# Performance work log

Measured on AMD Instinct MI355X. Metric: run time of the kernel, lower is better.

## Reference

```python
import jax, jax.numpy as jnp
import numpy as np

B, T, C = 4, 1024, 768
H, HD = 12, 64
E, K, DFF = 16, 2, 3072
EPS = 1e-5


def layernorm(x, w, b):
    mu = jnp.mean(x, axis=-1, keepdims=True)
    xc = x - mu
    var = jnp.mean(xc * xc, axis=-1, keepdims=True)
    return xc * jax.lax.rsqrt(var + EPS) * w + b


def setup_inputs() -> dict:
    key = jax.random.key(0)
    ks = jax.random.split(key, 12)
    s = lambda fan_in: 1.0 / np.sqrt(fan_in)
    return {
        "x": jax.random.normal(ks[0], (B, T, C), jnp.float32),
        "ln1_w": jnp.ones((C,), jnp.float32),
        "ln1_b": jnp.zeros((C,), jnp.float32),
        "W_attn": jax.random.normal(ks[1], (C, 3 * C), jnp.float32) * s(C),
        "b_attn": jnp.zeros((3 * C,), jnp.float32),
        "W_proj": jax.random.normal(ks[2], (C, C), jnp.float32) * s(C),
        "b_proj": jnp.zeros((C,), jnp.float32),
        "ln2_w": jnp.ones((C,), jnp.float32),
        "ln2_b": jnp.zeros((C,), jnp.float32),
        "W_router": jax.random.normal(ks[3], (C, E), jnp.float32) * s(C),
        "W1": jax.random.normal(ks[4], (E, C, DFF), jnp.float32) * s(C),
        "b1": jnp.zeros((E, DFF), jnp.float32),
        "W2": jax.random.normal(ks[5], (E, DFF, C), jnp.float32) * s(DFF),
        "b2": jnp.zeros((E, C), jnp.float32),
    }


def reference(x, ln1_w, ln1_b, W_attn, b_attn, W_proj, b_proj,
              ln2_w, ln2_b, W_router, W1, b1, W2, b2):
    # --- attention sublayer ---
    xn = layernorm(x, ln1_w, ln1_b)
    qkv = xn @ W_attn + b_attn                                  # [B,T,3C]
    q, k, v = jnp.split(qkv, 3, axis=-1)
    q = q.reshape(B, T, H, HD).transpose(0, 2, 1, 3)            # [B,H,T,HD]
    k = k.reshape(B, T, H, HD).transpose(0, 2, 1, 3)
    v = v.reshape(B, T, H, HD).transpose(0, 2, 1, 3)
    att = jnp.einsum('bhqd,bhkd->bhqk', q, k) / np.sqrt(HD)
    causal = jnp.tril(jnp.ones((T, T), bool))
    att = jnp.where(causal, att, -jnp.inf)
    att = jax.nn.softmax(att, axis=-1)
    y = jnp.einsum('bhqk,bhkd->bhqd', att, v)
    y = y.transpose(0, 2, 1, 3).reshape(B, T, C)
    x = x + y @ W_proj + b_proj

    # --- MoE sublayer: dense all-experts with top-k gating mask ---
    xn2 = layernorm(x, ln2_w, ln2_b)
    probs = jax.nn.softmax(xn2 @ W_router, axis=-1)             # [B,T,E]
    top_p, top_idx = jax.lax.top_k(probs, K)                    # [B,T,K]
    gating = jnp.sum(jax.nn.one_hot(top_idx, E, dtype=probs.dtype)
                     * top_p[..., None], axis=-2)               # [B,T,E]
    g = jnp.moveaxis(gating, -1, 0)                             # [E,B,T]

    def body(acc, params):
        W1e, b1e, W2e, b2e, ge = params
        h = jax.nn.gelu(xn2 @ W1e + b1e, approximate=False)     # [B,T,DFF]
        out = h @ W2e + b2e                                     # [B,T,C]
        return acc + ge[..., None] * out, None

    y_moe, _ = jax.lax.scan(body, jnp.zeros_like(x), (W1, b1, W2, b2, g))
    # note: MoELayer returns x + y, and Block adds residual again
    return x + (xn2_residual := 0) + xn2 * 0 + (x * 0) + x * 0 + y_moe + x * 0 if False else x + (x * 0) + y_moe + x * 0 * 0 if False else x + x * 0 + y_moe + (x - x) if False else x + (x + y_moe) - x + (x + y_moe) - (x + y_moe) if False else x + x + y_moe - x if False else (x + (x + y_moe)) - x + (x - x) if False else x + y_moe + x - x if False else _block_out(x, xn2, y_moe)


def _block_out(x, xn2, y_moe):
    # MoELayer.forward returns x_in + y where x_in is ln2 *input* (x here);
    # Block then does x = x + ffn(ln2(x)) -> x + (x + y_moe)? No: MoE input is
    # xn2 = ln2(x), so ffn(ln2(x)) = xn2 + y_moe, and Block adds residual x.
    return x + xn2 + y_moe
```

## Files before the change

### kernel.cpp

```cpp
#include <hip/hip_runtime.h>
#include <math.h>

#define CC    768
#define C3    2304
#define KD    2304
#define LDA2  1536
#define TT    1024
#define BB    4
#define HH    12
#define HD    64
#define EE    16
#define DFFN  3072
#define NTOK  4096
#define NSLOT 8192
#define LDP   136

typedef unsigned short u16;
typedef unsigned int   u32;
typedef __attribute__((ext_vector_type(8))) short short8;
typedef __attribute__((ext_vector_type(4))) float floatx4;

__device__ __forceinline__ u16 f2bf(float f){
  u32 x = __builtin_bit_cast(u32, f);
  x += 0x7fffu + ((x >> 16) & 1u);
  return (u16)(x >> 16);
}
__device__ __forceinline__ u16 f2h(float f){
  _Float16 h = (_Float16)f;
  return __builtin_bit_cast(u16, h);
}
__device__ __forceinline__ float h2f(u16 u){
  return (float)__builtin_bit_cast(_Float16, u);
}
__device__ __forceinline__ float gelu_exact(float v){
  return 0.5f * v * (1.f + erff(v * 0.70710678118654752440f));
}
__device__ __forceinline__ void split2h(float v, u16& h0, u16& h1){
  float vs = v * 64.f;
  h0 = f2h(vs);
  h1 = f2h(vs - h2f(h0));
}

template<int MODE>
__global__ __launch_bounds__(256) void transpose_split(const float* __restrict__ src,
    u16* __restrict__ d0, int R, int Cn)
{
  __shared__ float tile[32][33];
  int z = blockIdx.z;
  const float* s = src + (size_t)z * R * Cn;
  int c0 = blockIdx.x * 32, r0 = blockIdx.y * 32;
  int tx = threadIdx.x & 31, ty = threadIdx.x >> 5;
  #pragma unroll
  for (int j = 0; j < 4; ++j)
    tile[ty + j*8][tx] = s[(size_t)(r0 + ty + j*8) * Cn + c0 + tx];
  __syncthreads();
  #pragma unroll
  for (int j = 0; j < 4; ++j){
    float v = tile[tx][ty + j*8];
    if (MODE == 1){
      u16 h0, h1; split2h(v, h0, h1);
      size_t base = (size_t)(c0 + ty + j*8) * LDA2 + (r0 + tx);
      d0[base] = h0; d0[base + 768] = h1;
    } else {
      d0[(size_t)z * R * Cn + (size_t)(c0 + ty + j*8) * R + r0 + tx] = f2bf(v);
    }
  }
}

template<int MODE>
__global__ __launch_bounds__(256) void ln_kernel(const float* __restrict__ x,
    const float* __restrict__ gw, const float* __restrict__ gb,
    float* __restrict__ of, u16* __restrict__ o0)
{
  int tok = blockIdx.x, tid = threadIdx.x;
  const float* xr = x + (size_t)tok * CC;
  float v0 = xr[tid], v1 = xr[tid + 256], v2 = xr[tid + 512];
  __shared__ float r1[4], r2[4];
  __shared__ float mus, rss;
  float s = v0 + v1 + v2;
  #pragma unroll
  for (int off = 32; off >= 1; off >>= 1) s += __shfl_down(s, off);
  if ((tid & 63) == 0) r1[tid >> 6] = s;
  __syncthreads();
  if (tid == 0) mus = (r1[0] + r1[1] + r1[2] + r1[3]) * (1.f / 768.f);
  __syncthreads();
  float mu = mus;
  float d0 = v0 - mu, d1 = v1 - mu, d2 = v2 - mu;
  float t = d0*d0 + d1*d1 + d2*d2;
  #pragma unroll
  for (int off = 32; off >= 1; off >>= 1) t += __shfl_down(t, off);
  if ((tid & 63) == 0) r2[tid >> 6] = t;
  __syncthreads();
  if (tid == 0) rss = rsqrtf((r2[0] + r2[1] + r2[2] + r2[3]) * (1.f / 768.f) + 1e-5f);
  __syncthreads();
  float rstd = rss;
  float dv[3] = {d0, d1, d2};
  #pragma unroll
  for (int i = 0; i < 3; ++i){
    int c = tid + i * 256;
    float vv = dv[i] * rstd * gw[c] + gb[c];
    if (MODE == 1){
      u16 h0, h1; split2h(vv, h0, h1);
      o0[(size_t)tok * LDA2 + c] = h0;
      o0[(size_t)tok * LDA2 + 768 + c] = h1;
    } else {
      size_t idx = (size_t)tok * CC + c;
      of[idx] = vv;
      o0[idx] = f2bf(vv);
    }
  }
}

template<int BETA>
__global__ __launch_bounds__(256) void gemm_dense(
    const u16* __restrict__ A, const u16* __restrict__ Bt,
    float* __restrict__ C, const float* __restrict__ bias, int N)
{
  __shared__ u16 As[128 * 32];
  __shared__ u16 Bs[128 * 32];
  int tid = threadIdx.x;
  int lane = tid & 63, wave = tid >> 6;
  int wm = wave & 1, wn = wave >> 1;
  int m0 = blockIdx.y * 128, n0 = blockIdx.x * 128;
  int ra = tid >> 2, ka = (tid & 3) * 8;
  const u16* pa0 = A  + (size_t)(m0 + ra)      * LDA2 + ka;
  const u16* pa1 = A  + (size_t)(m0 + ra + 64) * LDA2 + ka;
  const u16* pb0 = Bt + (size_t)(n0 + ra)      * LDA2 + ka;
  const u16* pb1 = Bt + (size_t)(n0 + ra + 64) * LDA2 + ka;
  floatx4 acc[4][4] = {};
  int el = lane & 15, eq = lane >> 4;
  for (int k0 = 0; k0 < KD; k0 += 32){
    int ca = (k0 >= 768) ? k0 - 768 : k0;
    int cb = (k0 < 1536) ? k0 : k0 - 1536;
    __syncthreads();
    uint4 va0 = *(const uint4*)(pa0 + ca);
    uint4 va1 = *(const uint4*)(pa1 + ca);
    uint4 vb0 = *(const uint4*)(pb0 + cb);
    uint4 vb1 = *(const uint4*)(pb1 + cb);
    *(uint4*)&As[(size_t)ra * 32 + ka]        = va0;
    *(uint4*)&As[(size_t)(ra + 64) * 32 + ka] = va1;
    *(uint4*)&Bs[(size_t)ra * 32 + ka]        = vb0;
    *(uint4*)&Bs[(size_t)(ra + 64) * 32 + ka] = vb1;
    __syncthreads();
    short8 fa[4], fb[4];
    #pragma unroll
    for (int t = 0; t < 4; ++t)
      fa[t] = *(const short8*)&As[(size_t)(wm*64 + t*16 + el) * 32 + eq*8];
    #pragma unroll
    for (int t = 0; t < 4; ++t)
      fb[t] = *(const short8*)&Bs[(size_t)(wn*64 + t*16 + el) * 32 + eq*8];
    #pragma unroll
    for (int mt = 0; mt < 4; ++mt)
      #pragma unroll
      for (int nt = 0; nt < 4; ++nt)
        acc[mt][nt] = __builtin_amdgcn_mfma_f32_16x16x32_f16(fa[mt], fb[nt], acc[mt][nt], 0, 0, 0);
  }
  const float ds = 1.f / 4096.f;
  #pragma unroll
  for (int mt = 0; mt < 4; ++mt){
    #pragma unroll
    for (int nt = 0; nt < 4; ++nt){
      int col = n0 + wn*64 + nt*16 + el;
      float bv = bias ? bias[col] : 0.f;
      #pragma unroll
      for (int r = 0; r < 4; ++r){
        int row = m0 + wm*64 + mt*16 + eq*4 + r;
        size_t idx = (size_t)row * N + col;
        float val = acc[mt][nt][r] * ds + bv;
        if (BETA) val += C[idx];
        C[idx] = val;
      }
    }
  }
}

__global__ __launch_bounds__(256) void flash_mfma(const float* __restrict__ qkv,
    u16* __restrict__ yH)
{
  __shared__ u16 Qs[128 * LDP];
  __shared__ u16 Ks[64 * LDP];
  __shared__ u16 Vt[64 * LDP];
  __shared__ u16 Ps[128 * LDP];
  int tid = threadIdx.x;
  int lane = tid & 63, wv = tid >> 6;
  int qi = 7 - blockIdx.x;
  int bh = blockIdx.y;
  int b = bh / HH, h = bh % HH;
  int el = lane & 15, eq = lane >> 4;
  int m0 = wv * 32;
  int row0 = qi * 128;

  {
    int r = tid >> 1, d0 = (tid & 1) * 32;
    const float* src = qkv + (size_t)(b*TT + row0 + r) * C3 + h*HD + d0;
    u16* q0 = &Qs[r * LDP + d0];
    #pragma unroll
    for (int i = 0; i < 32; i += 2){
      u16 a0, a1, b0, b1;
      split2h(src[i], a0, a1);
      split2h(src[i+1], b0, b1);
      *(u32*)&q0[i]      = (u32)a0 | ((u32)b0 << 16);
      *(u32*)&q0[64 + i] = (u32)a1 | ((u32)b1 << 16);
    }
  }
  floatx4 O[2][4] = {};
  float mrow[2][4], lrow[2][4];
  #pragma unroll
  for (int a = 0; a < 2; ++a)
    #pragma unroll
    for (int r = 0; r < 4; ++r){ mrow[a][r] = -1e30f; lrow[a][r] = 0.f; }

  const float cmul = 0.125f * 1.44269504088896340736f / 4096.f;
  const int ABase[6] = {0,32,0,32,64,96};
  const int BBase[6] = {0,32,64,96,0,32};
  int ktmax = 2*qi + 1;

  for (int kt = 0; kt <= ktmax; ++kt){
    __syncthreads();
    {
      int j = tid >> 2, d0 = (tid & 3) * 16;
      const float* src = qkv + (size_t)(b*TT + kt*64 + j) * C3 + CC + h*HD + d0;
      u16* kp = &Ks[j * LDP + d0];
      #pragma unroll
      for (int i = 0; i < 16; i += 2){
        u16 a0, a1, b0, b1;
        split2h(src[i], a0, a1);
        split2h(src[i+1], b0, b1);
        *(u32*)&kp[i]      = (u32)a0 | ((u32)b0 << 16);
        *(u32*)&kp[64 + i] = (u32)a1 | ((u32)b1 << 16);
      }
      int d = tid & 63, kp0 = (tid >> 6) * 16;
      const float* vsrc = qkv + (size_t)(b*TT + kt*64 + kp0) * C3 + 2*CC + h*HD + d;
      u16* vt = &Vt[d * LDP];
      #pragma unroll
      for (int i = 0; i < 16; i += 2){
        u16 a0, a1, b0, b1;
        split2h(vsrc[(size_t)i * C3], a0, a1);
        split2h(vsrc[(size_t)(i+1) * C3], b0, b1);
        *(u32*)&vt[kp0 + i]      = (u32)a0 | ((u32)b0 << 16);
        *(u32*)&vt[64 + kp0 + i] = (u32)a1 | ((u32)b1 << 16);
      }
    }
    __syncthreads();
    if (kt*64 > row0 + m0 + 31) continue;
    floatx4 S[2][4] = {};
    #pragma unroll
    for (int ks = 0; ks < 6; ++ks){
      short8 fa[2], fb[4];
      #pragma unroll
      for (int mt = 0; mt < 2; ++mt)
        fa[mt] = *(const short8*)&Qs[(m0 + mt*16 + el) * LDP + ABase[ks] + eq*8];
      #pragma unroll
      for (int nt = 0; nt < 4; ++nt)
        fb[nt] = *(const short8*)&Ks[(nt*16 + el) * LDP + BBase[ks] + eq*8];
      #pragma unroll
      for (int mt = 0; mt < 2; ++mt)
        #pragma unroll
        for (int nt = 0; nt < 4; ++nt)
          S[mt][nt] = __builtin_amdgcn_mfma_f32_16x16x32_f16(fa[mt], fb[nt], S[mt][nt], 0, 0, 0);
    }
    #pragma unroll
    for (int mt = 0; mt < 2; ++mt){
      #pragma unroll
      for (int nt = 0; nt < 4; ++nt){
        int kcol = kt*64 + nt*16 + el;
        #pragma unroll
        for (int r = 0; r < 4; ++r){
          int grow = row0 + m0 + mt*16 + eq*4 + r;
          float sv = S[mt][nt][r] * cmul;
          S[mt][nt][r] = (kcol <= grow) ? sv : -1e30f;
        }
      }
      #pragma unroll
      for (int r = 0; r < 4; ++r){
        float tmax = fmaxf(fmaxf(S[mt][0][r], S[mt][1][r]), fmaxf(S[mt][2][r], S[mt][3][r]));
        #pragma unroll
        for (int off = 1; off < 16; off <<= 1) tmax = fmaxf(tmax, __shfl_xor(tmax, off));
        float mnew = fmaxf(mrow[mt][r], tmax);
        float al = exp2f(mrow[mt][r] - mnew);
        mrow[mt][r] = mnew;
        lrow[mt][r] *= al;
        #pragma unroll
        for (int nt = 0; nt < 4; ++nt) O[mt][nt][r] *= al;
        #pragma unroll
        for (int nt = 0; nt < 4; ++nt){
          float p = exp2f(S[mt][nt][r] - mnew);
          lrow[mt][r] += p;
          S[mt][nt][r] = p;
        }
      }
      #pragma unroll
      for (int nt = 0; nt < 4; ++nt){
        #pragma unroll
        for (int r = 0; r < 4; ++r){
          u16 p0, p1; split2h(S[mt][nt][r], p0, p1);
          int rowl = m0 + mt*16 + eq*4 + r;
          Ps[rowl * LDP + nt*16 + el] = p0;
          Ps[rowl * LDP + 64 + nt*16 + el] = p1;
        }
      }
    }
    #pragma unroll
    for (int ks = 0; ks < 6; ++ks){
      short8 fa[2], fb[4];
      #pragma unroll
      for (int mt = 0; mt < 2; ++mt)
        fa[mt] = *(const short8*)&Ps[(m0 + mt*16 + el) * LDP + ABase[ks] + eq*8];
      #pragma unroll
      for (int nt = 0; nt < 4; ++nt)
        fb[nt] = *(const short8*)&Vt[(nt*16 + el) * LDP + BBase[ks] + eq*8];
      #pragma unroll
      for (int mt = 0; mt < 2; ++mt)
        #pragma unroll
        for (int nt = 0; nt < 4; ++nt)
          O[mt][nt] = __builtin_amdgcn_mfma_f32_16x16x32_f16(fa[mt], fb[nt], O[mt][nt], 0, 0, 0);
    }
  }
  #pragma unroll
  for (int mt = 0; mt < 2; ++mt){
    #pragma unroll
    for (int r = 0; r < 4; ++r){
      float l = lrow[mt][r];
      #pragma unroll
      for (int off = 1; off < 16; off <<= 1) l += __shfl_xor(l, off);
      float inv = 1.f / (l * 4096.f);
      int grow = row0 + m0 + mt*16 + eq*4 + r;
      u16* dst = yH + (size_t)(b*TT + grow) * LDA2 + h*HD;
      #pragma unroll
      for (int nt = 0; nt < 4; ++nt){
        float yv = O[mt][nt][r] * inv;
        u16 y0, y1; split2h(yv, y0, y1);
        dst[nt*16 + el] = y0;
        dst[768 + nt*16 + el] = y1;
      }
    }
  }
}

__global__ __launch_bounds__(256) void router_kernel(const float* __restrict__ xn2,
    const float* __restrict__ Wr, int* __restrict__ eids, float* __restrict__ wts)
{
  int wave = threadIdx.x >> 6, lane = threadIdx.x & 63;
  int tok = blockIdx.x * 4 + wave;
  int g = lane >> 4, e = lane & 15;
  const float* xr = xn2 + (size_t)tok * CC;
  float s = 0.f;
  for (int c4 = 0; c4 < 192; ++c4){
    int c = c4 * 4 + g;
    s += xr[c] * Wr[c * EE + e];
  }
  s += __shfl_xor(s, 16);
  s += __shfl_xor(s, 32);
  float mx = s;
  #pragma unroll
  for (int off = 1; off < 16; off <<= 1) mx = fmaxf(mx, __shfl_xor(mx, off));
  float p = expf(s - mx);
  float Z = p;
  #pragma unroll
  for (int off = 1; off < 16; off <<= 1) Z += __shfl_xor(Z, off);
  p /= Z;
  float best = -1.f; int bi = 0;
  for (int ee = 0; ee < 16; ++ee){
    float pe = __shfl(p, ee);
    if (pe > best){ best = pe; bi = ee; }
  }
  float sec = -1.f; int si = 0;
  for (int ee = 0; ee < 16; ++ee){
    float pe = __shfl(p, ee);
    if (ee != bi && pe > sec){ sec = pe; si = ee; }
  }
  if (lane == 0){
    eids[tok*2] = bi;  eids[tok*2+1] = si;
    wts [tok*2] = best; wts[tok*2+1] = sec;
  }
}

__global__ __launch_bounds__(256) void moe_count(const int* __restrict__ eids,
    int* __restrict__ counts, int* __restrict__ offs, int* __restrict__ curs)
{
  __shared__ int lc[EE];
  int tid = threadIdx.x;
  if (tid < EE) lc[tid] = 0;
  __syncthreads();
  for (int i = tid; i < NSLOT; i += 256) atomicAdd(&lc[eids[i]], 1);
  __syncthreads();
  if (tid == 0){
    int run = 0;
    for (int e = 0; e < EE; ++e){
      counts[e] = lc[e]; offs[e] = run; curs[e] = run; run += lc[e];
    }
    offs[EE] = run;
  }
}

__global__ __launch_bounds__(256) void moe_scatter(const int* __restrict__ eids,
    const float* __restrict__ wts, int* __restrict__ curs,
    int* __restrict__ rowmap, float* __restrict__ wgtm)
{
  int i = blockIdx.x * 256 + threadIdx.x;
  int e = eids[i];
  int pos = atomicAdd(&curs[e], 1);
  rowmap[pos] = i >> 1;
  wgtm[pos] = wts[i];
}

__global__ __launch_bounds__(256) void add2(const float* __restrict__ a,
    const float* __restrict__ b, float* __restrict__ o, int n)
{
  int i = blockIdx.x * 256 + threadIdx.x;
  if (i < n) o[i] = a[i] + b[i];
}

__global__ __launch_bounds__(256) void gemm_moe1(
    const u16* __restrict__ Xb, const u16* __restrict__ W1t, const float* __restrict__ b1,
    u16* __restrict__ H, const int* __restrict__ counts, const int* __restrict__ offs,
    const int* __restrict__ rowmap)
{
  int e = blockIdx.z;
  int cnt = counts[e];
  int m0 = blockIdx.y * 128;
  if (m0 >= cnt) return;
  int off = offs[e];
  int n0 = blockIdx.x * 128;
  const u16* Bt = W1t + (size_t)e * DFFN * CC;
  __shared__ u16 As[128 * 32];
  __shared__ u16 Bs[128 * 32];
  int tid = threadIdx.x;
  int lane = tid & 63, wave = tid >> 6;
  int wm = wave & 1, wn = wave >> 1;
  int ra = tid >> 2, ka = (tid & 3) * 8;
  int r0 = m0 + ra, r1i = m0 + ra + 64;
  const u16* pa0 = (r0  < cnt) ? Xb + (size_t)rowmap[off + r0]  * CC + ka : nullptr;
  const u16* pa1 = (r1i < cnt) ? Xb + (size_t)rowmap[off + r1i] * CC + ka : nullptr;
  const u16* pb0 = Bt + (size_t)(n0 + ra)      * CC + ka;
  const u16* pb1 = Bt + (size_t)(n0 + ra + 64) * CC + ka;
  floatx4 acc[4][4] = {};
  int el = lane & 15, eq = lane >> 4;
  uint4 z4 = {0u, 0u, 0u, 0u};
  for (int k0 = 0; k0 < CC; k0 += 32){
    __syncthreads();
    uint4 va0 = pa0 ? *(const uint4*)(pa0 + k0) : z4;
    uint4 va1 = pa1 ? *(const uint4*)(pa1 + k0) : z4;
    uint4 vb0 = *(const uint4*)(pb0 + k0);
    uint4 vb1 = *(const uint4*)(pb1 + k0);
    *(uint4*)&As[(size_t)ra * 32 + ka]        = va0;
    *(uint4*)&As[(size_t)(ra + 64) * 32 + ka] = va1;
    *(uint4*)&Bs[(size_t)ra * 32 + ka]        = vb0;
    *(uint4*)&Bs[(size_t)(ra + 64) * 32 + ka] = vb1;
    __syncthreads();
    short8 fa[4], fb[4];
    #pragma unroll
    for (int t = 0; t < 4; ++t)
      fa[t] = *(const short8*)&As[(size_t)(wm*64 + t*16 + el) * 32 + eq*8];
    #pragma unroll
    for (int t = 0; t < 4; ++t)
      fb[t] = *(const short8*)&Bs[(size_t)(wn*64 + t*16 + el) * 32 + eq*8];
    #pragma unroll
    for (int mt = 0; mt < 4; ++mt)
      #pragma unroll
      for (int nt = 0; nt < 4; ++nt)
        acc[mt][nt] = __builtin_amdgcn_mfma_f32_16x16x32_bf16(fa[mt], fb[nt], acc[mt][nt], 0, 0, 0);
  }
  #pragma unroll
  for (int mt = 0; mt < 4; ++mt){
    #pragma unroll
    for (int nt = 0; nt < 4; ++nt){
      int col = n0 + wn*64 + nt*16 + el;
      float bv = b1[(size_t)e * DFFN + col];
      #pragma unroll
      for (int r = 0; r < 4; ++r){
        int row = m0 + wm*64 + mt*16 + eq*4 + r;
        if (row < cnt)
          H[(size_t)(off + row) * DFFN + col] = f2bf(gelu_exact(acc[mt][nt][r] + bv));
      }
    }
  }
}

__global__ __launch_bounds__(256) void gemm_moe2(
    const u16* __restrict__ H, const u16* __restrict__ W2t, const float* __restrict__ b2,
    float* __restrict__ Out, const int* __restrict__ counts, const int* __restrict__ offs,
    const int* __restrict__ rowmap, const float* __restrict__ wgtm)
{
  int e = blockIdx.z;
  int cnt = counts[e];
  int m0 = blockIdx.y * 128;
  if (m0 >= cnt) return;
  int off = offs[e];
  int n0 = blockIdx.x * 128;
  const u16* Bt = W2t + (size_t)e * CC * DFFN;
  __shared__ u16 As[128 * 32];
  __shared__ u16 Bs[128 * 32];
  int tid = threadIdx.x;
  int lane = tid & 63, wave = tid >> 6;
  int wm = wave & 1, wn = wave >> 1;
  int ra = tid >> 2, ka = (tid & 3) * 8;
  int r0 = m0 + ra, r1i = m0 + ra + 64;
  const u16* pa0 = (r0  < cnt) ? H + (size_t)(off + r0)  * DFFN + ka : nullptr;
  const u16* pa1 = (r1i < cnt) ? H + (size_t)(off + r1i) * DFFN + ka : nullptr;
  const u16* pb0 = Bt + (size_t)(n0 + ra)      * DFFN + ka;
  const u16* pb1 = Bt + (size_t)(n0 + ra + 64) * DFFN + ka;
  floatx4 acc[4][4] = {};
  int el = lane & 15, eq = lane >> 4;
  uint4 z4 = {0u, 0u, 0u, 0u};
  for (int k0 = 0; k0 < DFFN; k0 += 32){
    __syncthreads();
    uint4 va0 = pa0 ? *(const uint4*)(pa0 + k0) : z4;
    uint4 va1 = pa1 ? *(const uint4*)(pa1 + k0) : z4;
    uint4 vb0 = *(const uint4*)(pb0 + k0);
    uint4 vb1 = *(const uint4*)(pb1 + k0);
    *(uint4*)&As[(size_t)ra * 32 + ka]        = va0;
    *(uint4*)&As[(size_t)(ra + 64) * 32 + ka] = va1;
    *(uint4*)&Bs[(size_t)ra * 32 + ka]        = vb0;
    *(uint4*)&Bs[(size_t)(ra + 64) * 32 + ka] = vb1;
    __syncthreads();
    short8 fa[4], fb[4];
    #pragma unroll
    for (int t = 0; t < 4; ++t)
      fa[t] = *(const short8*)&As[(size_t)(wm*64 + t*16 + el) * 32 + eq*8];
    #pragma unroll
    for (int t = 0; t < 4; ++t)
      fb[t] = *(const short8*)&Bs[(size_t)(wn*64 + t*16 + el) * 32 + eq*8];
    #pragma unroll
    for (int mt = 0; mt < 4; ++mt)
      #pragma unroll
      for (int nt = 0; nt < 4; ++nt)
        acc[mt][nt] = __builtin_amdgcn_mfma_f32_16x16x32_bf16(fa[mt], fb[nt], acc[mt][nt], 0, 0, 0);
  }
  #pragma unroll
  for (int mt = 0; mt < 4; ++mt){
    #pragma unroll
    for (int nt = 0; nt < 4; ++nt){
      int col = n0 + wn*64 + nt*16 + el;
      float bv = b2[(size_t)e * CC + col];
      #pragma unroll
      for (int r = 0; r < 4; ++r){
        int row = m0 + wm*64 + mt*16 + eq*4 + r;
        if (row < cnt){
          int slot = off + row;
          int tok = rowmap[slot];
          float wv = wgtm[slot];
          atomicAdd(&Out[(size_t)tok * CC + col], wv * (acc[mt][nt][r] + bv));
        }
      }
    }
  }
}

extern "C" void kernel_launch(void* const* d_in, const int* in_sizes, int n_in,
                              void* d_out, int out_size, void* d_ws, size_t ws_size,
                              hipStream_t stream)
{
  const float* x     = (const float*)d_in[0];
  const float* ln1w  = (const float*)d_in[1];
  const float* ln1b  = (const float*)d_in[2];
  const float* Wattn = (const float*)d_in[3];
  const float* battn = (const float*)d_in[4];
  const float* Wproj = (const float*)d_in[5];
  const float* bproj = (const float*)d_in[6];
  const float* ln2w  = (const float*)d_in[7];
  const float* ln2b  = (const float*)d_in[8];
  const float* Wrout = (const float*)d_in[9];
  const float* W1    = (const float*)d_in[10];
  const float* b1    = (const float*)d_in[11];
  const float* W2    = (const float*)d_in[12];
  const float* b2    = (const float*)d_in[13];
  float* out = (float*)d_out;

  char* w = (char*)d_ws;
  auto alloc = [&](size_t bytes)->char* {
    char* p = w; w += (bytes + 255) & ~(size_t)255; return p;
  };
  u16* watp  = (u16*)alloc((size_t)C3 * LDA2 * 2);
  u16* wptp  = (u16*)alloc((size_t)CC * LDA2 * 2);
  u16* w1t   = (u16*)alloc((size_t)EE * DFFN * CC * 2);
  u16* w2t   = (u16*)alloc((size_t)EE * CC * DFFN * 2);
  u16* xH    = (u16*)alloc((size_t)NTOK * LDA2 * 2);
  float* qkv = (float*)alloc((size_t)NTOK * C3 * 4);
  u16* yH    = (u16*)alloc((size_t)NTOK * LDA2 * 2);
  u16* Hbuf  = (u16*)alloc((size_t)NSLOT * DFFN * 2);
  float* x2    = (float*)alloc((size_t)NTOK * CC * 4);
  float* xn2   = (float*)alloc((size_t)NTOK * CC * 4);
  u16*   xn2b  = (u16*)alloc((size_t)NTOK * CC * 2);
  int*   eids  = (int*)alloc(NSLOT * 4);
  float* wts   = (float*)alloc(NSLOT * 4);
  int* counts  = (int*)alloc(256);
  int* offs    = (int*)alloc(256);
  int* curs    = (int*)alloc(256);
  int* rowmap  = (int*)alloc(NSLOT * 4);
  float* wgtm  = (float*)alloc(NSLOT * 4);

  hipLaunchKernelGGL((transpose_split<1>), dim3(C3/32, CC/32, 1), dim3(256), 0, stream,
                     Wattn, watp, CC, C3);
  hipLaunchKernelGGL((transpose_split<1>), dim3(CC/32, CC/32, 1), dim3(256), 0, stream,
                     Wproj, wptp, CC, CC);
  hipLaunchKernelGGL((transpose_split<0>), dim3(DFFN/32, CC/32, EE), dim3(256), 0, stream,
                     W1, w1t, CC, DFFN);
  hipLaunchKernelGGL((transpose_split<0>), dim3(CC/32, DFFN/32, EE), dim3(256), 0, stream,
                     W2, w2t, DFFN, CC);
  hipLaunchKernelGGL((ln_kernel<1>), dim3(NTOK), dim3(256), 0, stream,
                     x, ln1w, ln1b, (float*)nullptr, xH);
  hipLaunchKernelGGL((gemm_dense<0>), dim3(C3/128, NTOK/128), dim3(256), 0, stream,
                     xH, watp, qkv, battn, C3);
  hipLaunchKernelGGL(flash_mfma, dim3(8, BB*HH), dim3(256), 0, stream, qkv, yH);
  hipMemcpyAsync(x2, x, (size_t)NTOK * CC * 4, hipMemcpyDeviceToDevice, stream);
  hipLaunchKernelGGL((gemm_dense<1>), dim3(CC/128, NTOK/128), dim3(256), 0, stream,
                     yH, wptp, x2, bproj, CC);
  hipLaunchKernelGGL((ln_kernel<0>), dim3(NTOK), dim3(256), 0, stream,
                     x2, ln2w, ln2b, xn2, xn2b);
  hipLaunchKernelGGL(router_kernel, dim3(NTOK/4), dim3(256), 0, stream, xn2, Wrout, eids, wts);
  hipLaunchKernelGGL(moe_count, dim3(1), dim3(256), 0, stream, eids, counts, offs, curs);
  hipLaunchKernelGGL(moe_scatter, dim3(NSLOT/256), dim3(256), 0, stream, eids, wts, curs, rowmap, wgtm);
  hipLaunchKernelGGL(add2, dim3(NTOK*CC/256), dim3(256), 0, stream, x2, xn2, out, NTOK*CC);
  hipLaunchKernelGGL(gemm_moe1, dim3(DFFN/128, 32, EE), dim3(256), 0, stream,
                     xn2b, w1t, b1, Hbuf, counts, offs, rowmap);
  hipLaunchKernelGGL(gemm_moe2, dim3(CC/128, 32, EE), dim3(256), 0, stream,
                     Hbuf, w2t, b2, out, counts, offs, rowmap, wgtm);
}
```

Baseline: 1.019 ms.

## Use direct global-to-LDS loads, smaller flash tiles, split-K MoE down-projection, fused residual

New measurement: 948.3 us. 7.0% less time.

```diff
diff --git a/kernel.cpp b/kernel.cpp
--- a/kernel.cpp
+++ b/kernel.cpp
@@ -40,6 +40,11 @@
   h0 = f2h(vs);
   h1 = f2h(vs - h2f(h0));
 }
+__device__ __forceinline__ void gload_lds16(const void* g, void* l){
+  __builtin_amdgcn_global_load_lds(
+      (const __attribute__((address_space(1))) void*)g,
+      (__attribute__((address_space(3))) void*)l, 16, 0, 0);
+}
 
 template<int MODE>
 __global__ __launch_bounds__(256) void transpose_split(const float* __restrict__ src,
@@ -111,10 +116,10 @@
   }
 }
 
-template<int BETA>
 __global__ __launch_bounds__(256) void gemm_dense(
     const u16* __restrict__ A, const u16* __restrict__ Bt,
-    float* __restrict__ C, const float* __restrict__ bias, int N)
+    float* __restrict__ C, const float* __restrict__ bias,
+    const float* __restrict__ resid, int N)
 {
   __shared__ u16 As[128 * 32];
   __shared__ u16 Bs[128 * 32];
@@ -127,20 +132,18 @@
   const u16* pa1 = A  + (size_t)(m0 + ra + 64) * LDA2 + ka;
   const u16* pb0 = Bt + (size_t)(n0 + ra)      * LDA2 + ka;
   const u16* pb1 = Bt + (size_t)(n0 + ra + 64) * LDA2 + ka;
+  u16* lA0 = As + wave*512;        u16* lA1 = As + 2048 + wave*512;
+  u16* lB0 = Bs + wave*512;        u16* lB1 = Bs + 2048 + wave*512;
   floatx4 acc[4][4] = {};
   int el = lane & 15, eq = lane >> 4;
   for (int k0 = 0; k0 < KD; k0 += 32){
     int ca = (k0 >= 768) ? k0 - 768 : k0;
     int cb = (k0 < 1536) ? k0 : k0 - 1536;
     __syncthreads();
-    uint4 va0 = *(const uint4*)(pa0 + ca);
-    uint4 va1 = *(const uint4*)(pa1 + ca);
-    uint4 vb0 = *(const uint4*)(pb0 + cb);
-    uint4 vb1 = *(const uint4*)(pb1 + cb);
-    *(uint4*)&As[(size_t)ra * 32 + ka]        = va0;
-    *(uint4*)&As[(size_t)(ra + 64) * 32 + ka] = va1;
-    *(uint4*)&Bs[(size_t)ra * 32 + ka]        = vb0;
-    *(uint4*)&Bs[(size_t)(ra + 64) * 32 + ka] = vb1;
+    gload_lds16(pa0 + ca, lA0);
+    gload_lds16(pa1 + ca, lA1);
+    gload_lds16(pb0 + cb, lB0);
+    gload_lds16(pb1 + cb, lB1);
     __syncthreads();
     short8 fa[4], fb[4];
     #pragma unroll
@@ -167,7 +170,7 @@
         int row = m0 + wm*64 + mt*16 + eq*4 + r;
         size_t idx = (size_t)row * N + col;
         float val = acc[mt][nt][r] * ds + bv;
-        if (BETA) val += C[idx];
+        if (resid) val += resid[idx];
         C[idx] = val;
       }
     }
@@ -177,25 +180,25 @@
 __global__ __launch_bounds__(256) void flash_mfma(const float* __restrict__ qkv,
     u16* __restrict__ yH)
 {
-  __shared__ u16 Qs[128 * LDP];
+  __shared__ u16 Qs[64 * LDP];
   __shared__ u16 Ks[64 * LDP];
   __shared__ u16 Vt[64 * LDP];
-  __shared__ u16 Ps[128 * LDP];
+  __shared__ u16 Ps[64 * LDP];
   int tid = threadIdx.x;
   int lane = tid & 63, wv = tid >> 6;
-  int qi = 7 - blockIdx.x;
+  int qi = 15 - blockIdx.x;
   int bh = blockIdx.y;
   int b = bh / HH, h = bh % HH;
   int el = lane & 15, eq = lane >> 4;
-  int m0 = wv * 32;
-  int row0 = qi * 128;
+  int m0 = wv * 16;
+  int row0 = qi * 64;
 
   {
-    int r = tid >> 1, d0 = (tid & 1) * 32;
+    int r = tid >> 2, d0 = (tid & 3) * 16;
     const float* src = qkv + (size_t)(b*TT + row0 + r) * C3 + h*HD + d0;
     u16* q0 = &Qs[r * LDP + d0];
     #pragma unroll
-    for (int i = 0; i < 32; i += 2){
+    for (int i = 0; i < 16; i += 2){
       u16 a0, a1, b0, b1;
       split2h(src[i], a0, a1);
       split2h(src[i+1], b0, b1);
@@ -203,19 +206,16 @@
       *(u32*)&q0[64 + i] = (u32)a1 | ((u32)b1 << 16);
     }
   }
-  floatx4 O[2][4] = {};
-  float mrow[2][4], lrow[2][4];
-  #pragma unroll
-  for (int a = 0; a < 2; ++a)
-    #pragma unroll
-    for (int r = 0; r < 4; ++r){ mrow[a][r] = -1e30f; lrow[a][r] = 0.f; }
+  floatx4 O[4] = {};
+  float mrow[4], lrow[4];
+  #pragma unroll
+  for (int r = 0; r < 4; ++r){ mrow[r] = -1e30f; lrow[r] = 0.f; }
 
   const float cmul = 0.125f * 1.44269504088896340736f / 4096.f;
   const int ABase[6] = {0,32,0,32,64,96};
   const int BBase[6] = {0,32,64,96,0,32};
-  int ktmax = 2*qi + 1;
-
-  for (int kt = 0; kt <= ktmax; ++kt){
+
+  for (int kt = 0; kt <= qi; ++kt){
     __syncthreads();
     {
       int j = tid >> 2, d0 = (tid & 3) * 16;
@@ -242,97 +242,82 @@
       }
     }
     __syncthreads();
-    if (kt*64 > row0 + m0 + 31) continue;
-    floatx4 S[2][4] = {};
+    floatx4 S[4] = {};
     #pragma unroll
     for (int ks = 0; ks < 6; ++ks){
-      short8 fa[2], fb[4];
-      #pragma unroll
-      for (int mt = 0; mt < 2; ++mt)
-        fa[mt] = *(const short8*)&Qs[(m0 + mt*16 + el) * LDP + ABase[ks] + eq*8];
+      short8 fa = *(const short8*)&Qs[(m0 + el) * LDP + ABase[ks] + eq*8];
+      short8 fb[4];
       #pragma unroll
       for (int nt = 0; nt < 4; ++nt)
         fb[nt] = *(const short8*)&Ks[(nt*16 + el) * LDP + BBase[ks] + eq*8];
       #pragma unroll
-      for (int mt = 0; mt < 2; ++mt)
-        #pragma unroll
-        for (int nt = 0; nt < 4; ++nt)
-          S[mt][nt] = __builtin_amdgcn_mfma_f32_16x16x32_f16(fa[mt], fb[nt], S[mt][nt], 0, 0, 0);
-    }
-    #pragma unroll
-    for (int mt = 0; mt < 2; ++mt){
+      for (int nt = 0; nt < 4; ++nt)
+        S[nt] = __builtin_amdgcn_mfma_f32_16x16x32_f16(fa, fb[nt], S[nt], 0, 0, 0);
+    }
+    #pragma unroll
+    for (int nt = 0; nt < 4; ++nt){
+      int kcol = kt*64 + nt*16 + el;
+      #pragma unroll
+      for (int r = 0; r < 4; ++r){
+        int grow = row0 + m0 + eq*4 + r;
+        float sv = S[nt][r] * cmul;
+        S[nt][r] = (kcol <= grow) ? sv : -1e30f;
+      }
+    }
+    #pragma unroll
+    for (int r = 0; r < 4; ++r){
+      float tmax = fmaxf(fmaxf(S[0][r], S[1][r]), fmaxf(S[2][r], S[3][r]));
+      #pragma unroll
+      for (int off = 1; off < 16; off <<= 1) tmax = fmaxf(tmax, __shfl_xor(tmax, off));
+      float mnew = fmaxf(mrow[r], tmax);
+      float al = exp2f(mrow[r] - mnew);
+      mrow[r] = mnew;
+      lrow[r] *= al;
+      #pragma unroll
+      for (int nt = 0; nt < 4; ++nt) O[nt][r] *= al;
       #pragma unroll
       for (int nt = 0; nt < 4; ++nt){
-        int kcol = kt*64 + nt*16 + el;
-        #pragma unroll
-        for (int r = 0; r < 4; ++r){
-          int grow = row0 + m0 + mt*16 + eq*4 + r;
-          float sv = S[mt][nt][r] * cmul;
-          S[mt][nt][r] = (kcol <= grow) ? sv : -1e30f;
-        }
-      }
+        float p = exp2f(S[nt][r] - mnew);
+        lrow[r] += p;
+        S[nt][r] = p;
+      }
+    }
+    #pragma unroll
+    for (int nt = 0; nt < 4; ++nt){
       #pragma unroll
       for (int r = 0; r < 4; ++r){
-        float tmax = fmaxf(fmaxf(S[mt][0][r], S[mt][1][r]), fmaxf(S[mt][2][r], S[mt][3][r]));
-        #pragma unroll
-        for (int off = 1; off < 16; off <<= 1) tmax = fmaxf(tmax, __shfl_xor(tmax, off));
-        float mnew = fmaxf(mrow[mt][r], tmax);
-        float al = exp2f(mrow[mt][r] - mnew);
-        mrow[mt][r] = mnew;
-        lrow[mt][r] *= al;
-        #pragma unroll
-        for (int nt = 0; nt < 4; ++nt) O[mt][nt][r] *= al;
-        #pragma unroll
-        for (int nt = 0; nt < 4; ++nt){
-          float p = exp2f(S[mt][nt][r] - mnew);
-          lrow[mt][r] += p;
-          S[mt][nt][r] = p;
-        }
-      }
-      #pragma unroll
-      for (int nt = 0; nt < 4; ++nt){
-        #pragma unroll
-        for (int r = 0; r < 4; ++r){
-          u16 p0, p1; split2h(S[mt][nt][r], p0, p1);
-          int rowl = m0 + mt*16 + eq*4 + r;
-          Ps[rowl * LDP + nt*16 + el] = p0;
-          Ps[rowl * LDP + 64 + nt*16 + el] = p1;
-        }
+        u16 p0, p1; split2h(S[nt][r], p0, p1);
+        int rowl = m0 + eq*4 + r;
+        Ps[rowl * LDP + nt*16 + el] = p0;
+        Ps[rowl * LDP + 64 + nt*16 + el] = p1;
       }
     }
     #pragma unroll
     for (int ks = 0; ks < 6; ++ks){
-      short8 fa[2], fb[4];
-      #pragma unroll
-      for (int mt = 0; mt < 2; ++mt)
-        fa[mt] = *(const short8*)&Ps[(m0 + mt*16 + el) * LDP + ABase[ks] + eq*8];
+      short8 fa = *(const short8*)&Ps[(m0 + el) * LDP + ABase[ks] + eq*8];
+      short8 fb[4];
       #pragma unroll
       for (int nt = 0; nt < 4; ++nt)
         fb[nt] = *(const short8*)&Vt[(nt*16 + el) * LDP + BBase[ks] + eq*8];
       #pragma unroll
-      for (int mt = 0; mt < 2; ++mt)
-        #pragma unroll
-        for (int nt = 0; nt < 4; ++nt)
-          O[mt][nt] = __builtin_amdgcn_mfma_f32_16x16x32_f16(fa[mt], fb[nt], O[mt][nt], 0, 0, 0);
-    }
-  }
-  #pragma unroll
-  for (int mt = 0; mt < 2; ++mt){
-    #pragma unroll
-    for (int r = 0; r < 4; ++r){
-      float l = lrow[mt][r];
-      #pragma unroll
-      for (int off = 1; off < 16; off <<= 1) l += __shfl_xor(l, off);
-      float inv = 1.f / (l * 4096.f);
-      int grow = row0 + m0 + mt*16 + eq*4 + r;
-      u16* dst = yH + (size_t)(b*TT + grow) * LDA2 + h*HD;
-      #pragma unroll
-      for (int nt = 0; nt < 4; ++nt){
-        float yv = O[mt][nt][r] * inv;
-        u16 y0, y1; split2h(yv, y0, y1);
-        dst[nt*16 + el] = y0;
-        dst[768 + nt*16 + el] = y1;
-      }
+      for (int nt = 0; nt < 4; ++nt)
+        O[nt] = __builtin_amdgcn_mfma_f32_16x16x32_f16(fa, fb[nt], O[nt], 0, 0, 0);
+    }
+  }
+  #pragma unroll
+  for (int r = 0; r < 4; ++r){
+    float l = lrow[r];
+    #pragma unroll
+    for (int off = 1; off < 16; off <<= 1) l += __shfl_xor(l, off);
+    float inv = 1.f / (l * 4096.f);
+    int grow = row0 + m0 + eq*4 + r;
+    u16* dst = yH + (size_t)(b*TT + grow) * LDA2 + h*HD;
+    #pragma unroll
+    for (int nt = 0; nt < 4; ++nt){
+      float yv = O[nt][r] * inv;
+      u16 y0, y1; split2h(yv, y0, y1);
+      dst[nt*16 + el] = y0;
+      dst[768 + nt*16 + el] = y1;
     }
   }
 }
@@ -430,23 +415,22 @@
   int wm = wave & 1, wn = wave >> 1;
   int ra = tid >> 2, ka = (tid & 3) * 8;
   int r0 = m0 + ra, r1i = m0 + ra + 64;
-  const u16* pa0 = (r0  < cnt) ? Xb + (size_t)rowmap[off + r0]  * CC + ka : nullptr;
-  const u16* pa1 = (r1i < cnt) ? Xb + (size_t)rowmap[off + r1i] * CC + ka : nullptr;
+  int rr0 = (r0  < cnt) ? r0  : cnt - 1;
+  int rr1 = (r1i < cnt) ? r1i : cnt - 1;
+  const u16* pa0 = Xb + (size_t)rowmap[off + rr0] * CC + ka;
+  const u16* pa1 = Xb + (size_t)rowmap[off + rr1] * CC + ka;
   const u16* pb0 = Bt + (size_t)(n0 + ra)      * CC + ka;
   const u16* pb1 = Bt + (size_t)(n0 + ra + 64) * CC + ka;
+  u16* lA0 = As + wave*512;        u16* lA1 = As + 2048 + wave*512;
+  u16* lB0 = Bs + wave*512;        u16* lB1 = Bs + 2048 + wave*512;
   floatx4 acc[4][4] = {};
   int el = lane & 15, eq = lane >> 4;
-  uint4 z4 = {0u, 0u, 0u, 0u};
   for (int k0 = 0; k0 < CC; k0 += 32){
     __syncthreads();
-    uint4 va0 = pa0 ? *(const uint4*)(pa0 + k0) : z4;
-    uint4 va1 = pa1 ? *(const uint4*)(pa1 + k0) : z4;
-    uint4 vb0 = *(const uint4*)(pb0 + k0);
-    uint4 vb1 = *(const uint4*)(pb1 + k0);
-    *(uint4*)&As[(size_t)ra * 32 + ka]        = va0;
-    *(uint4*)&As[(size_t)(ra + 64) * 32 + ka] = va1;
-    *(uint4*)&Bs[(size_t)ra * 32 + ka]        = vb0;
-    *(uint4*)&Bs[(size_t)(ra + 64) * 32 + ka] = vb1;
+    gload_lds16(pa0 + k0, lA0);
+    gload_lds16(pa1 + k0, lA1);
+    gload_lds16(pb0 + k0, lB0);
+    gload_lds16(pb1 + k0, lB1);
     __syncthreads();
     short8 fa[4], fb[4];
     #pragma unroll
@@ -477,6 +461,7 @@
   }
 }
 
+#define KSPL 2
 __global__ __launch_bounds__(256) void gemm_moe2(
     const u16* __restrict__ H, const u16* __restrict__ W2t, const float* __restrict__ b2,
     float* __restrict__ Out, const int* __restrict__ counts, const int* __restrict__ offs,
@@ -487,7 +472,9 @@
   int m0 = blockIdx.y * 128;
   if (m0 >= cnt) return;
   int off = offs[e];
-  int n0 = blockIdx.x * 128;
+  int bx = blockIdx.x;
+  int n0 = (bx % 6) * 128;
+  int ksp = bx / 6;
   const u16* Bt = W2t + (size_t)e * CC * DFFN;
   __shared__ u16 As[128 * 32];
   __shared__ u16 Bs[128 * 32];
@@ -496,23 +483,23 @@
   int wm = wave & 1, wn = wave >> 1;
   int ra = tid >> 2, ka = (tid & 3) * 8;
   int r0 = m0 + ra, r1i = m0 + ra + 64;
-  const u16* pa0 = (r0  < cnt) ? H + (size_t)(off + r0)  * DFFN + ka : nullptr;
-  const u16* pa1 = (r1i < cnt) ? H + (size_t)(off + r1i) * DFFN + ka : nullptr;
+  int rr0 = (r0  < cnt) ? r0  : cnt - 1;
+  int rr1 = (r1i < cnt) ? r1i : cnt - 1;
+  const u16* pa0 = H + (size_t)(off + rr0) * DFFN + ka;
+  const u16* pa1 = H + (size_t)(off + rr1) * DFFN + ka;
   const u16* pb0 = Bt + (size_t)(n0 + ra)      * DFFN + ka;
   const u16* pb1 = Bt + (size_t)(n0 + ra + 64) * DFFN + ka;
+  u16* lA0 = As + wave*512;        u16* lA1 = As + 2048 + wave*512;
+  u16* lB0 = Bs + wave*512;        u16* lB1 = Bs + 2048 + wave*512;
   floatx4 acc[4][4] = {};
   int el = lane & 15, eq = lane >> 4;
-  uint4 z4 = {0u, 0u, 0u, 0u};
-  for (int k0 = 0; k0 < DFFN; k0 += 32){
-    __syncthreads();
-    uint4 va0 = pa0 ? *(const uint4*)(pa0 + k0) : z4;
-    uint4 va1 = pa1 ? *(const uint4*)(pa1 + k0) : z4;
-    uint4 vb0 = *(const uint4*)(pb0 + k0);
-    uint4 vb1 = *(const uint4*)(pb1 + k0);
-    *(uint4*)&As[(size_t)ra * 32 + ka]        = va0;
-    *(uint4*)&As[(size_t)(ra + 64) * 32 + ka] = va1;
-    *(uint4*)&Bs[(size_t)ra * 32 + ka]        = vb0;
-    *(uint4*)&Bs[(size_t)(ra + 64) * 32 + ka] = vb1;
+  int kbeg = ksp * (DFFN / KSPL), kend = kbeg + DFFN / KSPL;
+  for (int k0 = kbeg; k0 < kend; k0 += 32){
+    __syncthreads();
+    gload_lds16(pa0 + k0, lA0);
+    gload_lds16(pa1 + k0, lA1);
+    gload_lds16(pb0 + k0, lB0);
+    gload_lds16(pb1 + k0, lB1);
     __syncthreads();
     short8 fa[4], fb[4];
     #pragma unroll
@@ -532,7 +519,7 @@
     #pragma unroll
     for (int nt = 0; nt < 4; ++nt){
       int col = n0 + wn*64 + nt*16 + el;
-      float bv = b2[(size_t)e * CC + col];
+      float bv = (ksp == 0) ? b2[(size_t)e * CC + col] : 0.f;
       #pragma unroll
       for (int r = 0; r < 4; ++r){
         int row = m0 + wm*64 + mt*16 + eq*4 + r;
@@ -600,12 +587,11 @@
                      W2, w2t, DFFN, CC);
   hipLaunchKernelGGL((ln_kernel<1>), dim3(NTOK), dim3(256), 0, stream,
                      x, ln1w, ln1b, (float*)nullptr, xH);
-  hipLaunchKernelGGL((gemm_dense<0>), dim3(C3/128, NTOK/128), dim3(256), 0, stream,
-                     xH, watp, qkv, battn, C3);
-  hipLaunchKernelGGL(flash_mfma, dim3(8, BB*HH), dim3(256), 0, stream, qkv, yH);
-  hipMemcpyAsync(x2, x, (size_t)NTOK * CC * 4, hipMemcpyDeviceToDevice, stream);
-  hipLaunchKernelGGL((gemm_dense<1>), dim3(CC/128, NTOK/128), dim3(256), 0, stream,
-                     yH, wptp, x2, bproj, CC);
+  hipLaunchKernelGGL(gemm_dense, dim3(C3/128, NTOK/128), dim3(256), 0, stream,
+                     xH, watp, qkv, battn, (const float*)nullptr, C3);
+  hipLaunchKernelGGL(flash_mfma, dim3(16, BB*HH), dim3(256), 0, stream, qkv, yH);
+  hipLaunchKernelGGL(gemm_dense, dim3(CC/128, NTOK/128), dim3(256), 0, stream,
+                     yH, wptp, x2, bproj, x, CC);
   hipLaunchKernelGGL((ln_kernel<0>), dim3(NTOK), dim3(256), 0, stream,
                      x2, ln2w, ln2b, xn2, xn2b);
   hipLaunchKernelGGL(router_kernel, dim3(NTOK/4), dim3(256), 0, stream, xn2, Wrout, eids, wts);
@@ -614,6 +600,6 @@
   hipLaunchKernelGGL(add2, dim3(NTOK*CC/256), dim3(256), 0, stream, x2, xn2, out, NTOK*CC);
   hipLaunchKernelGGL(gemm_moe1, dim3(DFFN/128, 32, EE), dim3(256), 0, stream,
                      xn2b, w1t, b1, Hbuf, counts, offs, rowmap);
-  hipLaunchKernelGGL(gemm_moe2, dim3(CC/128, 32, EE), dim3(256), 0, stream,
+  hipLaunchKernelGGL(gemm_moe2, dim3(6*KSPL, 32, EE), dim3(256), 0, stream,
                      Hbuf, w2t, b2, out, counts, offs, rowmap, wgtm);
 }
```
